# Kernel tuning notes

Measured on AMD Instinct MI355X. Metric: run time of the kernel, lower is better.

Reference implementation:

```python
import jax, jax.numpy as jnp
import numpy as np

EPS = 1e-5


def _gcn_conv(x, src, dst, norm, W, b, n_nodes):
    # PyG GCNConv: transform, then normalized scatter-add aggregation (self-loops included in src/dst)
    h = x @ W                                   # [N, out]
    msg = h[src] * norm[:, None]                # gather over edges [E+N, out]
    agg = jax.ops.segment_sum(msg, dst, num_segments=n_nodes)
    return agg + b


def _bn(x, gamma, beta):
    # BatchNorm1d in training mode: batch stats over node axis, biased variance
    mu = jnp.mean(x, axis=0)
    var = jnp.mean((x - mu) ** 2, axis=0)
    return (x - mu) * jax.lax.rsqrt(var + EPS) * gamma + beta


def setup_inputs() -> dict:
    key = jax.random.key(0)
    ks = jax.random.split(key, 8)
    N, E, F_in, H, F_out = 50000, 800000, 32, 96, 2
    x = jax.random.normal(ks[0], (N, F_in), dtype=jnp.float32)
    edge_index = jax.random.randint(ks[1], (2, E), 0, N, dtype=jnp.int64)
    def lin(k, fi, fo):
        s = 1.0 / np.sqrt(fi)
        return jax.random.uniform(k, (fi, fo), jnp.float32, -s, s)
    W1 = lin(ks[2], F_in, H); b1 = jnp.zeros((H,), jnp.float32)
    W2 = lin(ks[3], H, H);    b2 = jnp.zeros((H,), jnp.float32)
    W3 = lin(ks[4], H, H);    b3 = jnp.zeros((H,), jnp.float32)
    W4 = lin(ks[5], H, F_out); b4 = jnp.zeros((F_out,), jnp.float32)
    g1 = jnp.ones((H,), jnp.float32); be1 = jnp.zeros((H,), jnp.float32)
    g2 = jnp.ones((H,), jnp.float32); be2 = jnp.zeros((H,), jnp.float32)
    g3 = jnp.ones((H,), jnp.float32); be3 = jnp.zeros((H,), jnp.float32)
    return dict(x=x, edge_index=edge_index,
                W1=W1, b1=b1, g1=g1, be1=be1,
                W2=W2, b2=b2, g2=g2, be2=be2,
                W3=W3, b3=b3, g3=g3, be3=be3,
                W4=W4, b4=b4)


def reference(x, edge_index, W1, b1, g1, be1, W2, b2, g2, be2, W3, b3, g3, be3, W4, b4):
    N = x.shape[0]
    loop = jnp.arange(N, dtype=edge_index.dtype)
    src = jnp.concatenate([edge_index[0], loop])   # add self-loops
    dst = jnp.concatenate([edge_index[1], loop])
    deg = jax.ops.segment_sum(jnp.ones_like(dst, dtype=x.dtype), dst, num_segments=N)
    dinv = jnp.where(deg > 0, jax.lax.rsqrt(deg), 0.0)
    norm = dinv[src] * dinv[dst]                   # D^{-1/2} (A+I) D^{-1/2}

    h = jax.nn.relu(_bn(_gcn_conv(x, src, dst, norm, W1, b1, N), g1, be1))
    h = jax.nn.relu(_bn(_gcn_conv(h, src, dst, norm, W2, b2, N), g2, be2))
    h = jax.nn.relu(_bn(_gcn_conv(h, src, dst, norm, W3, b3, N), g3, be3))
    return _gcn_conv(h, src, dst, norm, W4, b4, N)
```

## Files before the change

kernel.cpp:

```cpp
#include <hip/hip_runtime.h>
#include <hip/hip_bf16.h>

using bf16x8 = __attribute__((ext_vector_type(8))) short;
using f32x4  = __attribute__((ext_vector_type(4))) float;

#define FS_CHUNK 4096

__device__ __forceinline__ float ldf(const void* p, size_t i, float isf){
  if (isf > 0.5f) return ((const float*)p)[i];
  unsigned int u = ((unsigned int)((const unsigned short*)p)[i]) << 16;
  return __uint_as_float(u);
}
__device__ __forceinline__ unsigned short f2bf(float v){
  unsigned int u = __float_as_uint(v);
  u = (u + 0x7FFFu + ((u >> 16) & 1u)) >> 16;
  return (unsigned short)u;
}
__device__ __forceinline__ unsigned int pk2(float a, float b){
  return (unsigned int)f2bf(a) | ((unsigned int)f2bf(b) << 16);
}
__device__ __forceinline__ float lo16(unsigned int u){ return __uint_as_float(u << 16); }
__device__ __forceinline__ float hi16(unsigned int u){ return __uint_as_float(u & 0xFFFF0000u); }

template<typename IT>
__device__ __forceinline__ void load8idx(const IT* p, int* o){
  if (sizeof(IT) == 2){
    uint4 v = *(const uint4*)p;
    o[0] = (int)(v.x & 0xFFFFu); o[1] = (int)(v.x >> 16);
    o[2] = (int)(v.y & 0xFFFFu); o[3] = (int)(v.y >> 16);
    o[4] = (int)(v.z & 0xFFFFu); o[5] = (int)(v.z >> 16);
    o[6] = (int)(v.w & 0xFFFFu); o[7] = (int)(v.w >> 16);
  } else {
    int4 a = ((const int4*)p)[0];
    int4 c = ((const int4*)p)[1];
    o[0]=a.x; o[1]=a.y; o[2]=a.z; o[3]=a.w;
    o[4]=c.x; o[5]=c.y; o[6]=c.z; o[7]=c.w;
  }
}

__global__ void k_fill(unsigned short* o, unsigned short v, int n){
  int i = blockIdx.x*blockDim.x + threadIdx.x;
  if (i < n) o[i] = v;
}

__global__ void k_prep(const unsigned short* xh, const unsigned int* eu,
                       float* flag, int nelemX, long long E,
                       const void* W1, const void* W2, const void* W3, const void* W4,
                       unsigned short* __restrict__ Wt1, unsigned short* __restrict__ Wt2,
                       unsigned short* __restrict__ Wt3, float* __restrict__ W4f,
                       int* __restrict__ cnt, float* __restrict__ stAll,
                       unsigned short* __restrict__ HS, int n){
  int t = threadIdx.x;
  if (blockIdx.x > 0){
    if (blockIdx.x == 1 && t < 96) HS[(size_t)96*n + t] = 0;
    int total = n + 4609;
    for (int i = (int)(blockIdx.x-1)*256 + t; i < total; i += (int)(gridDim.x-1)*256){
      if (i < n) cnt[i] = 0; else stAll[i - n] = 0.f;
    }
    return;
  }
  __shared__ int sf32, si64;
  __shared__ float sisf;
  if (t == 0){ sf32 = 0; si64 = 1; }
  __syncthreads();
  {
    int i = 2*t;
    if (i < nelemX){
      unsigned e8 = (xh[i] >> 7) & 0xFFu;
      if (e8 >= 140u) sf32 = 1;
    }
    if ((long long)(2*t + 1) < 2*E){
      if (eu[2*t + 1] != 0u) si64 = 0;
    }
  }
  __syncthreads();
  if (t == 0){
    flag[0] = (float)sf32; flag[1] = (float)si64;
    sisf = (float)sf32;
  }
  __syncthreads();
  float isf = sisf;
  for (int q = t; q < 3072; q += 256){
    int nn = q >> 5, k = q & 31;
    Wt1[q] = f2bf(ldf(W1, (size_t)96*k + nn, isf));
  }
  for (int q = t; q < 9216; q += 256){
    int nn = q/96, k = q - 96*nn;
    Wt2[q] = f2bf(ldf(W2, (size_t)96*k + nn, isf));
    Wt3[q] = f2bf(ldf(W3, (size_t)96*k + nn, isf));
  }
  if (t < 192) W4f[t] = ldf(W4, t, isf);
}

__global__ void k_cnt2p(const int* __restrict__ ei, const float* __restrict__ flag,
                        int* __restrict__ cnt, unsigned int* __restrict__ ec,
                        long long E, int n){
  long long i = (long long)blockIdx.x*blockDim.x + threadIdx.x;
  long long i0 = 2*i;
  if (i0 >= E) return;
  bool i64 = (flag[1] > 0.5f);
  bool two = (i0 + 1 < E);
  int s0, d0, s1 = 0, d1 = -1;
  if ((E & 1LL) == 0){
    if (i64){
      uint4 vs = ((const uint4*)ei)[i];
      uint4 vd = ((const uint4*)(ei + 2*E))[i];
      s0 = (int)vs.x; s1 = (int)vs.z; d0 = (int)vd.x; d1 = (int)vd.z;
    } else {
      int2 vs = ((const int2*)ei)[i];
      int2 vd = ((const int2*)(ei + E))[i];
      s0 = vs.x; s1 = vs.y; d0 = vd.x; d1 = vd.y;
    }
  } else {
    if (i64){ s0 = ei[2*i0]; d0 = ei[2*E + 2*i0];
              if (two){ s1 = ei[2*i0+2]; d1 = ei[2*E + 2*i0 + 2]; } }
    else    { s0 = ei[i0];   d0 = ei[E + i0];
              if (two){ s1 = ei[i0+1];   d1 = ei[E + i0 + 1]; } }
  }
  bool ok0 = ((unsigned)s0 < (unsigned)n) && ((unsigned)d0 < (unsigned)n);
  bool ok1 = two && ((unsigned)s1 < (unsigned)n) && ((unsigned)d1 < (unsigned)n);
  unsigned p0 = ok0 ? (((unsigned)d0 << 16) | (unsigned)s0) : 0xFFFFFFFFu;
  unsigned p1 = ok1 ? (((unsigned)d1 << 16) | (unsigned)s1) : 0xFFFFFFFFu;
  if (two){
    uint2 o; o.x = p0; o.y = p1;
    ((uint2*)ec)[i] = o;
  } else {
    ec[i0] = p0;
  }
  if (ok0) atomicAdd(&cnt[d0], 1);
  if (ok1) atomicAdd(&cnt[d1], 1);
}

__global__ void k_cnt2(const int* __restrict__ ei, const float* __restrict__ flag,
                       int* __restrict__ cnt, int* __restrict__ ec,
                       long long E, int n){
  long long i = (long long)blockIdx.x*blockDim.x + threadIdx.x;
  long long i0 = 2*i;
  if (i0 >= E) return;
  bool i64 = (flag[1] > 0.5f);
  bool two = (i0 + 1 < E);
  int s0, d0, s1 = 0, d1 = -1;
  if ((E & 1LL) == 0){
    if (i64){
      uint4 vs = ((const uint4*)ei)[i];
      uint4 vd = ((const uint4*)(ei + 2*E))[i];
      s0 = (int)vs.x; s1 = (int)vs.z; d0 = (int)vd.x; d1 = (int)vd.z;
    } else {
      int2 vs = ((const int2*)ei)[i];
      int2 vd = ((const int2*)(ei + E))[i];
      s0 = vs.x; s1 = vs.y; d0 = vd.x; d1 = vd.y;
    }
  } else {
    if (i64){ s0 = ei[2*i0]; d0 = ei[2*E + 2*i0];
              if (two){ s1 = ei[2*i0+2]; d1 = ei[2*E + 2*i0 + 2]; } }
    else    { s0 = ei[i0];   d0 = ei[E + i0];
              if (two){ s1 = ei[i0+1];   d1 = ei[E + i0 + 1]; } }
  }
  bool ok0 = ((unsigned)s0 < (unsigned)n) && ((unsigned)d0 < (unsigned)n);
  bool ok1 = two && ((unsigned)s1 < (unsigned)n) && ((unsigned)d1 < (unsigned)n);
  if (!ok0){ s0 = -1; d0 = -1; }
  if (!ok1){ s1 = -1; d1 = -1; }
  if (two){
    int4 o; o.x = s0; o.y = d0; o.z = s1; o.w = d1;
    ((int4*)ec)[i] = o;
  } else {
    int2 o; o.x = s0; o.y = d0;
    ((int2*)ec)[i0] = o;
  }
  if (ok0) atomicAdd(&cnt[d0], 1);
  if (ok1) atomicAdd(&cnt[d1], 1);
}

template<typename IT>
__global__ void k_emit2(const int* __restrict__ cnt, int* __restrict__ gctr,
                        int* __restrict__ rowst, int* __restrict__ cursor,
                        float* __restrict__ dinv, IT* __restrict__ csr, int n){
  int i = blockIdx.x*256 + threadIdx.x;
  int lane = threadIdx.x & 63;
  int v  = (i < n) ? cnt[i] : 0;
  int rv = (v + 7) & ~7;
  int s = rv;
  #pragma unroll
  for (int off = 1; off < 64; off <<= 1){
    int u = __shfl_up(s, off, 64);
    if (lane >= off) s += u;
  }
  int wtot = __shfl(s, 63, 64);
  int base = 0;
  if (lane == 63) base = atomicAdd(gctr, wtot);
  base = __shfl(base, 63, 64);
  if (i < n){
    int r = base + s - rv;
    rowst[i]  = r;
    cursor[i] = r;
    dinv[i]   = rsqrtf((float)(1 + v));
    for (int p = r + v; p < r + rv; ++p) csr[p] = (IT)n;
  }
}

__global__ __launch_bounds__(256) void k_fxp(const unsigned int* __restrict__ ec,
      int* __restrict__ cursor, unsigned short* __restrict__ csr,
      long long E, int n, int gF8,
      const void* __restrict__ x, const float* __restrict__ flag,
      const float* __restrict__ dinv, unsigned short* __restrict__ XS){
  int t = threadIdx.x;
  if ((int)blockIdx.x < gF8){
    int part = blockIdx.x & 7;
    long long base = (long long)(blockIdx.x >> 3) * FS_CHUNK;
    int pl = (int)(((long long)n *  part     ) >> 3);
    int pr = (int)(((long long)n * (part + 1)) >> 3);
    long long lim = base + FS_CHUNK < E ? base + FS_CHUNK : E;
    for (long long i = base + 4*t; i < lim; i += 1024){
      uint4 v = ((const uint4*)ec)[i >> 2];
      { int d = (int)(v.x >> 16);
        if (d >= pl && d < pr){ int p = atomicAdd(&cursor[d], 1); csr[p] = (unsigned short)(v.x & 0xFFFFu); } }
      if (i + 1 < lim){ int d = (int)(v.y >> 16);
        if (d >= pl && d < pr){ int p = atomicAdd(&cursor[d], 1); csr[p] = (unsigned short)(v.y & 0xFFFFu); } }
      if (i + 2 < lim){ int d = (int)(v.z >> 16);
        if (d >= pl && d < pr){ int p = atomicAdd(&cursor[d], 1); csr[p] = (unsigned short)(v.z & 0xFFFFu); } }
      if (i + 3 < lim){ int d = (int)(v.w >> 16);
        if (d >= pl && d < pr){ int p = atomicAdd(&cursor[d], 1); csr[p] = (unsigned short)(v.w & 0xFFFFu); } }
    }
    return;
  }
  int q = (int)(blockIdx.x - gF8)*256 + t;
  if (q < 4*(n+1)){
    int node = q >> 2, part = q & 3;
    uint4 o;
    if (node < n){
      float isf = flag[0];
      float di = dinv[node];
      if (isf > 0.5f){
        const float* xr = (const float*)x + (size_t)32*node + 8*part;
        o.x = pk2(xr[0]*di, xr[1]*di); o.y = pk2(xr[2]*di, xr[3]*di);
        o.z = pk2(xr[4]*di, xr[5]*di); o.w = pk2(xr[6]*di, xr[7]*di);
      } else {
        uint4 v = ((const uint4*)x)[(size_t)4*node + part];
        o.x = pk2(lo16(v.x)*di, hi16(v.x)*di);
        o.y = pk2(lo16(v.y)*di, hi16(v.y)*di);
        o.z = pk2(lo16(v.z)*di, hi16(v.z)*di);
        o.w = pk2(lo16(v.w)*di, hi16(v.w)*di);
      }
    } else { o.x = o.y = o.z = o.w = 0u; }
    ((uint4*)XS)[q] = o;
  }
}

__global__ __launch_bounds__(256) void k_fx(const int* __restrict__ ec,
      int* __restrict__ cursor, int* __restrict__ csr,
      long long E, int n, int gF8,
      const void* __restrict__ x, const float* __restrict__ flag,
      const float* __restrict__ dinv, unsigned short* __restrict__ XS){
  int t = threadIdx.x;
  if ((int)blockIdx.x < gF8){
    int part = blockIdx.x & 7;
    long long base = (long long)(blockIdx.x >> 3) * FS_CHUNK;
    int pl = (int)(((long long)n *  part     ) >> 3);
    int pr = (int)(((long long)n * (part + 1)) >> 3);
    long long lim = base + FS_CHUNK < E ? base + FS_CHUNK : E;
    for (long long i = base + 2*t; i < lim; i += 512){
      int4 v = ((const int4*)ec)[i >> 1];
      if (v.y >= pl && v.y < pr && (unsigned)v.x < (unsigned)n){
        int p = atomicAdd(&cursor[v.y], 1);
        csr[p] = v.x;
      }
      if (i + 1 < lim && v.w >= pl && v.w < pr && (unsigned)v.z < (unsigned)n){
        int p = atomicAdd(&cursor[v.w], 1);
        csr[p] = v.z;
      }
    }
    return;
  }
  int q = (int)(blockIdx.x - gF8)*256 + t;
  if (q < 4*(n+1)){
    int node = q >> 2, part = q & 3;
    uint4 o;
    if (node < n){
      float isf = flag[0];
      float di = dinv[node];
      if (isf > 0.5f){
        const float* xr = (const float*)x + (size_t)32*node + 8*part;
        o.x = pk2(xr[0]*di, xr[1]*di); o.y = pk2(xr[2]*di, xr[3]*di);
        o.z = pk2(xr[4]*di, xr[5]*di); o.w = pk2(xr[6]*di, xr[7]*di);
      } else {
        uint4 v = ((const uint4*)x)[(size_t)4*node + part];
        o.x = pk2(lo16(v.x)*di, hi16(v.x)*di);
        o.y = pk2(lo16(v.y)*di, hi16(v.y)*di);
        o.z = pk2(lo16(v.z)*di, hi16(v.z)*di);
        o.w = pk2(lo16(v.w)*di, hi16(v.w)*di);
      }
    } else { o.x = o.y = o.z = o.w = 0u; }
    ((uint4*)XS)[q] = o;
  }
}

#define ACC8(v) { a0+=lo16((v).x); a1+=hi16((v).x); a2+=lo16((v).y); a3+=hi16((v).y); \
                  a4+=lo16((v).z); a5+=hi16((v).z); a6+=lo16((v).w); a7+=hi16((v).w); }

template<typename IT>
__global__ __launch_bounds__(256) void k_aggx(const uint4* __restrict__ xs4,
      const int* __restrict__ rowst, const int* __restrict__ cnt,
      const IT* __restrict__ csr, const float* __restrict__ dinv,
      const unsigned short* __restrict__ Wt1b,
      unsigned short* __restrict__ Zb, float* __restrict__ stout, int n){
  __shared__ __align__(16) unsigned short Xs[64][40];
  __shared__ __align__(16) unsigned short Wt[96][40];
  __shared__ float bs[96], bq[96];
  int t = threadIdx.x;
  for (int q = t; q < 384; q += 256){
    uint4 v = ((const uint4*)Wt1b)[q];
    *(uint4*)&Wt[q >> 2][(q & 3)*8] = v;
  }
  if (t < 96){ bs[t] = 0.f; bq[t] = 0.f; }
  int g = t & 3, ty = t >> 2;
  int node = blockIdx.x*64 + ty;
  float a0=0.f,a1=0.f,a2=0.f,a3=0.f,a4=0.f,a5=0.f,a6=0.f,a7=0.f;
  if (node < n){
    uint4 v = xs4[(size_t)node*4 + g];
    ACC8(v);
    int bq_ = rowst[node];
    int bnd = bq_ + ((cnt[node] + 7) & ~7);
    for (int j = bq_; j < bnd; j += 8){
      int ix[8];
      load8idx<IT>(csr + j, ix);
      uint4 v0 = xs4[(size_t)ix[0]*4 + g];
      uint4 v1 = xs4[(size_t)ix[1]*4 + g];
      uint4 v2 = xs4[(size_t)ix[2]*4 + g];
      uint4 v3 = xs4[(size_t)ix[3]*4 + g];
      uint4 v4 = xs4[(size_t)ix[4]*4 + g];
      uint4 v5 = xs4[(size_t)ix[5]*4 + g];
      uint4 v6 = xs4[(size_t)ix[6]*4 + g];
      uint4 v7 = xs4[(size_t)ix[7]*4 + g];
      ACC8(v0); ACC8(v1); ACC8(v2); ACC8(v3);
      ACC8(v4); ACC8(v5); ACC8(v6); ACC8(v7);
    }
    float di = dinv[node];
    a0*=di; a1*=di; a2*=di; a3*=di; a4*=di; a5*=di; a6*=di; a7*=di;
  }
  uint4 o;
  o.x = pk2(a0,a1); o.y = pk2(a2,a3); o.z = pk2(a4,a5); o.w = pk2(a6,a7);
  *(uint4*)&Xs[ty][8*g] = o;
  __syncthreads();
  int wv = t >> 6, lane = t & 63;
  int m = lane & 15, quad = lane >> 4;
  bf16x8 av = *(const bf16x8*)&Xs[16*wv + m][8*quad];
  f32x4 acc[6];
  #pragma unroll
  for (int c = 0; c < 6; ++c) acc[c] = (f32x4)(0.f);
  #pragma unroll
  for (int c = 0; c < 6; ++c){
    bf16x8 bv = *(const bf16x8*)&Wt[16*c + m][8*quad];
    acc[c] = __builtin_amdgcn_mfma_f32_16x16x32_bf16(av, bv, acc[c], 0, 0, 0);
  }
  int rowbase = blockIdx.x*64 + 16*wv + 4*quad;
  #pragma unroll
  for (int c = 0; c < 6; ++c){
    int col = 16*c + m;
    float s = 0.f, q = 0.f;
    #pragma unroll
    for (int r = 0; r < 4; ++r){
      int rr = rowbase + r;
      if (rr < n){
        unsigned short h = f2bf(acc[c][r]);
        Zb[(size_t)96*rr + col] = h;
        float br = __uint_as_float(((unsigned int)h) << 16);
        s += br; q += br*br;
      }
    }
    atomicAdd(&bs[col], s);
    atomicAdd(&bq[col], q);
  }
  __syncthreads();
  if (t < 96){
    int rep = blockIdx.x & 7;
    atomicAdd(&stout[192*rep + t],      bs[t]);
    atomicAdd(&stout[192*rep + 96 + t], bq[t]);
  }
}

template<typename IT>
__global__ __launch_bounds__(192) void k_agg(const uint4* __restrict__ hsr,
      const int* __restrict__ rowst, const int* __restrict__ cnt,
      const IT* __restrict__ csr,
      const float* __restrict__ dinv, uint4* __restrict__ zb4,
      float* __restrict__ stout, int n){
  __shared__ float ls[16][97], lq[16][97];
  int g = threadIdx.x, ty = threadIdx.y;
  int t = ty*12 + g;
  int node = blockIdx.x*16 + ty;
  float r[8];
  if (node < n){
    uint4 v = hsr[(size_t)node*12 + g];
    float a0 = lo16(v.x), a1 = hi16(v.x), a2 = lo16(v.y), a3 = hi16(v.y);
    float a4 = lo16(v.z), a5 = hi16(v.z), a6 = lo16(v.w), a7 = hi16(v.w);
    int bq_ = rowst[node];
    int bnd = bq_ + ((cnt[node] + 7) & ~7);
    for (int j = bq_; j < bnd; j += 8){
      int ix[8];
      load8idx<IT>(csr + j, ix);
      uint4 v0 = hsr[(size_t)ix[0]*12 + g];
      uint4 v1 = hsr[(size_t)ix[1]*12 + g];
      uint4 v2 = hsr[(size_t)ix[2]*12 + g];
      uint4 v3 = hsr[(size_t)ix[3]*12 + g];
      uint4 v4 = hsr[(size_t)ix[4]*12 + g];
      uint4 v5 = hsr[(size_t)ix[5]*12 + g];
      uint4 v6 = hsr[(size_t)ix[6]*12 + g];
      uint4 v7 = hsr[(size_t)ix[7]*12 + g];
      ACC8(v0); ACC8(v1); ACC8(v2); ACC8(v3);
      ACC8(v4); ACC8(v5); ACC8(v6); ACC8(v7);
    }
    float di = dinv[node];
    uint4 o;
    o.x = pk2(a0*di, a1*di);
    o.y = pk2(a2*di, a3*di);
    o.z = pk2(a4*di, a5*di);
    o.w = pk2(a6*di, a7*di);
    zb4[(size_t)node*12 + g] = o;
    r[0]=lo16(o.x); r[1]=hi16(o.x); r[2]=lo16(o.y); r[3]=hi16(o.y);
    r[4]=lo16(o.z); r[5]=hi16(o.z); r[6]=lo16(o.w); r[7]=hi16(o.w);
  } else {
    #pragma unroll
    for (int jj = 0; jj < 8; ++jj) r[jj] = 0.f;
  }
  #pragma unroll
  for (int jj = 0; jj < 8; ++jj){
    ls[ty][8*g + jj] = r[jj];
    lq[ty][8*g + jj] = r[jj]*r[jj];
  }
  __syncthreads();
  if (t < 96){
    float s = 0.f, q = 0.f;
    #pragma unroll
    for (int rr = 0; rr < 16; ++rr){ s += ls[rr][t]; q += lq[rr][t]; }
    int rep = blockIdx.x & 7;
    atomicAdd(&stout[192*rep + t],      s);
    atomicAdd(&stout[192*rep + 96 + t], q);
  }
}

__global__ __launch_bounds__(256) void k_linm(const unsigned short* __restrict__ zb,
      const unsigned short* __restrict__ Wtb, const float* __restrict__ st,
      const void* __restrict__ gam, const void* __restrict__ bet,
      const float* __restrict__ flag, const float* __restrict__ dinv,
      unsigned short* __restrict__ HS, int n, float invN){
  __shared__ float sa[96], sc[96];
  __shared__ __align__(16) unsigned short Ys[64][104];
  __shared__ __align__(16) unsigned short Wt[96][104];
  int t = threadIdx.x;
  if (t < 96){
    float ssum = 0.f, qsum = 0.f;
    #pragma unroll
    for (int r = 0; r < 8; ++r){ ssum += st[192*r + t]; qsum += st[192*r + 96 + t]; }
    float isf = flag[0];
    float mu  = ssum*invN;
    float var = fmaxf(qsum*invN - mu*mu, 0.f);
    float istd = rsqrtf(var + 1e-5f);
    float a = ldf(gam, t, isf)*istd;
    sa[t] = a; sc[t] = ldf(bet, t, isf) - mu*a;
  }
  for (int q = t; q < 1152; q += 256){
    uint4 v = ((const uint4*)Wtb)[q];
    *(uint4*)&Wt[q/12][8*(q - 12*(q/12))] = v;
  }
  __syncthreads();
  {
    int row = t >> 2, part = t & 3;
    int node = blockIdx.x*64 + row;
    if (node < n){
      const uint4* zr = (const uint4*)(zb + (size_t)96*node) + 3*part;
      #pragma unroll
      for (int q = 0; q < 3; ++q){
        uint4 zz = zr[q];
        int k = 24*part + 8*q;
        float y0 = fmaxf(lo16(zz.x)*sa[k]   + sc[k],   0.f);
        float y1 = fmaxf(hi16(zz.x)*sa[k+1] + sc[k+1], 0.f);
        float y2 = fmaxf(lo16(zz.y)*sa[k+2] + sc[k+2], 0.f);
        float y3 = fmaxf(hi16(zz.y)*sa[k+3] + sc[k+3], 0.f);
        float y4 = fmaxf(lo16(zz.z)*sa[k+4] + sc[k+4], 0.f);
        float y5 = fmaxf(hi16(zz.z)*sa[k+5] + sc[k+5], 0.f);
        float y6 = fmaxf(lo16(zz.w)*sa[k+6] + sc[k+6], 0.f);
        float y7 = fmaxf(hi16(zz.w)*sa[k+7] + sc[k+7], 0.f);
        *(unsigned int*)&Ys[row][k]     = pk2(y0, y1);
        *(unsigned int*)&Ys[row][k + 2] = pk2(y2, y3);
        *(unsigned int*)&Ys[row][k + 4] = pk2(y4, y5);
        *(unsigned int*)&Ys[row][k + 6] = pk2(y6, y7);
      }
    } else {
      unsigned int* yp = (unsigned int*)&Ys[row][24*part];
      #pragma unroll
      for (int q = 0; q < 12; ++q) yp[q] = 0u;
    }
  }
  __syncthreads();
  int wv = t >> 6, lane = t & 63;
  int m = lane & 15, quad = lane >> 4;
  bf16x8 av[3];
  #pragma unroll
  for (int kt = 0; kt < 3; ++kt)
    av[kt] = *(const bf16x8*)&Ys[16*wv + m][32*kt + 8*quad];
  f32x4 acc[6];
  #pragma unroll
  for (int c = 0; c < 6; ++c) acc[c] = (f32x4)(0.f);
  #pragma unroll
  for (int c = 0; c < 6; ++c){
    const unsigned short* wrow = &Wt[16*c + m][8*quad];
    #pragma unroll
    for (int kt = 0; kt < 3; ++kt){
      bf16x8 bv = *(const bf16x8*)(wrow + 32*kt);
      acc[c] = __builtin_amdgcn_mfma_f32_16x16x32_bf16(av[kt], bv, acc[c], 0, 0, 0);
    }
  }
  int rowbase = blockIdx.x*64 + 16*wv + 4*quad;
  float div[4];
  #pragma unroll
  for (int r = 0; r < 4; ++r){ int rr = rowbase + r; div[r] = (rr < n) ? dinv[rr] : 0.f; }
  #pragma unroll
  for (int c = 0; c < 6; ++c){
    int col = 16*c + m;
    #pragma unroll
    for (int r = 0; r < 4; ++r){
      int rr = rowbase + r;
      if (rr < n) HS[(size_t)96*rr + col] = f2bf(acc[c][r]*div[r]);
    }
  }
}

__global__ __launch_bounds__(256) void k_lin4(const unsigned short* __restrict__ zb,
      const float* __restrict__ Wf, const float* __restrict__ st,
      const void* __restrict__ gam, const void* __restrict__ bet,
      const float* __restrict__ flag, const float* __restrict__ dinv,
      float* __restrict__ hs2, int n, float invN){
  __shared__ float sa[96], sc[96];
  int t = threadIdx.x;
  if (t < 96){
    float ssum = 0.f, qsum = 0.f;
    #pragma unroll
    for (int r = 0; r < 8; ++r){ ssum += st[192*r + t]; qsum += st[192*r + 96 + t]; }
    float isf = flag[0];
    float mu  = ssum*invN;
    float var = fmaxf(qsum*invN - mu*mu, 0.f);
    float istd = rsqrtf(var + 1e-5f);
    float a = ldf(gam, t, isf)*istd;
    sa[t] = a; sc[t] = ldf(bet, t, isf) - mu*a;
  }
  __syncthreads();
  int i = blockIdx.x*blockDim.x + t;
  if (i >= n) return;
  const uint4* zr = (const uint4*)(zb + (size_t)96*i);
  float a0 = 0.f, a1 = 0.f;
  #pragma unroll
  for (int q = 0; q < 12; ++q){
    uint4 zz = zr[q];
    int k = 8*q;
    float y;
    y = fmaxf(lo16(zz.x)*sa[k]   + sc[k],   0.f); a0 += y*Wf[2*k];    a1 += y*Wf[2*k+1];
    y = fmaxf(hi16(zz.x)*sa[k+1] + sc[k+1], 0.f); a0 += y*Wf[2*k+2];  a1 += y*Wf[2*k+3];
    y = fmaxf(lo16(zz.y)*sa[k+2] + sc[k+2], 0.f); a0 += y*Wf[2*k+4];  a1 += y*Wf[2*k+5];
    y = fmaxf(hi16(zz.y)*sa[k+3] + sc[k+3], 0.f); a0 += y*Wf[2*k+6];  a1 += y*Wf[2*k+7];
    y = fmaxf(lo16(zz.z)*sa[k+4] + sc[k+4], 0.f); a0 += y*Wf[2*k+8];  a1 += y*Wf[2*k+9];
    y = fmaxf(hi16(zz.z)*sa[k+5] + sc[k+5], 0.f); a0 += y*Wf[2*k+10]; a1 += y*Wf[2*k+11];
    y = fmaxf(lo16(zz.w)*sa[k+6] + sc[k+6], 0.f); a0 += y*Wf[2*k+12]; a1 += y*Wf[2*k+13];
    y = fmaxf(hi16(zz.w)*sa[k+7] + sc[k+7], 0.f); a0 += y*Wf[2*k+14]; a1 += y*Wf[2*k+15];
  }
  float di = dinv[i];
  hs2[(size_t)2*i]   = di*a0;
  hs2[(size_t)2*i+1] = di*a1;
}

template<typename IT>
__global__ void k_agg2(const float2* __restrict__ hs2, const int* __restrict__ rowst,
                       const int* __restrict__ cnt, const IT* __restrict__ csr,
                       const float* __restrict__ dinv,
                       const void* __restrict__ b4, const float* __restrict__ flag,
                       void* __restrict__ out, int n){
  int node = blockIdx.x*blockDim.x + threadIdx.x;
  if (node >= n) return;
  float2 a = hs2[node];
  int b = rowst[node], e = b + cnt[node];
  int j = b;
  for (; j + 3 < e; j += 4){
    float2 v0 = hs2[(size_t)csr[j]];
    float2 v1 = hs2[(size_t)csr[j+1]];
    float2 v2 = hs2[(size_t)csr[j+2]];
    float2 v3 = hs2[(size_t)csr[j+3]];
    a.x += v0.x + v1.x + v2.x + v3.x;
    a.y += v0.y + v1.y + v2.y + v3.y;
  }
  for (; j < e; ++j){
    float2 v = hs2[(size_t)csr[j]];
    a.x += v.x; a.y += v.y;
  }
  float isf = flag[0];
  float di = dinv[node];
  float v0 = a.x*di + ldf(b4, 0, isf);
  float v1 = a.y*di + ldf(b4, 1, isf);
  if (isf > 0.5f){
    ((float*)out)[(size_t)2*node]   = v0;
    ((float*)out)[(size_t)2*node+1] = v1;
  } else {
    ((unsigned short*)out)[(size_t)2*node]   = f2bf(v0);
    ((unsigned short*)out)[(size_t)2*node+1] = f2bf(v1);
  }
}

extern "C" void kernel_launch(void* const* d_in, const int* in_sizes, int n_in,
                              void* d_out, int out_size, void* d_ws, size_t ws_size,
                              hipStream_t stream)
{
  const int B = 256;
  unsigned short* outh = (unsigned short*)d_out;

  if (n_in < 16){
    k_fill<<<(out_size+B-1)/B, B, 0, stream>>>(outh, 0x3F40u, out_size); return;
  }
  const int N = in_sizes[0] / 32;
  const long long E = in_sizes[1] / 2;
  if (in_sizes[0] % 32 != 0 || out_size != 2*N){
    k_fill<<<(out_size+B-1)/B, B, 0, stream>>>(outh, 0x3F60u, out_size); return;
  }
  const bool u16 = (N < 65536);

  size_t Npad = ((size_t)N + 3) & ~(size_t)3;
  float* ws   = (float*)d_ws;
  float* dinv = ws;
  float* hs2  = dinv + Npad;
  float* flag = hs2 + (size_t)2*N;
  float* stAll= flag + 4;
  float* W4f  = stAll + 4612;
  unsigned short* Wt1b = (unsigned short*)(W4f + 192);
  unsigned short* Wt2b = Wt1b + 3072;
  unsigned short* Wt3b = Wt2b + 9216;
  int* cnt    = (int*)(Wt3b + 9216);
  int* cursor = cnt + N;
  int* rowst  = cursor + N;
  uintptr_t cs_ = (uintptr_t)(rowst + N);
  cs_ = (cs_ + 15) & ~(uintptr_t)15;
  void* csrv  = (void*)cs_;
  size_t csrCap = (size_t)E + 8*(size_t)N;
  size_t csrBytes = csrCap * (u16 ? 2 : 4);
  uintptr_t hp_ = cs_ + csrBytes;
  hp_ = (hp_ + 15) & ~(uintptr_t)15;
  unsigned short* HS = (unsigned short*)hp_;
  unsigned short* Zb = HS + (size_t)96*(N+1);
  uintptr_t ec_ = (uintptr_t)(Zb + (size_t)96*N);
  ec_ = (ec_ + 15) & ~(uintptr_t)15;
  void* ecv = (void*)ec_;

  size_t ecBytes = u16 ? ((size_t)E + 4)*4 : ((size_t)2*E + 4)*4;
  size_t needB = (ec_ + ecBytes - (uintptr_t)d_ws) + 64;
  if (ws_size < needB){
    k_fill<<<(out_size+B-1)/B, B, 0, stream>>>(outh, 0x3F00u, out_size); return;
  }

  unsigned short* XS = HS;

  const void* x  = d_in[0];
  const int*  ei = (const int*)d_in[1];
  const void* W1 = d_in[2];
  const void* g1 = d_in[4];  const void* be1 = d_in[5];
  const void* W2 = d_in[6];
  const void* g2 = d_in[8];  const void* be2 = d_in[9];
  const void* W3 = d_in[10];
  const void* g3 = d_in[12]; const void* be3 = d_in[13];
  const void* W4 = d_in[14];
  const void* b4 = d_in[15];

  float* stA = stAll;
  float* stB = stAll + 1536;
  float* stC = stAll + 3072;
  int*   gctr = (int*)(stAll + 4608);

  int gN  = (N + B - 1)/B;
  long long hE = (E + 1)/2;
  int gE2 = (int)((hE + B - 1)/B); if (gE2 < 1) gE2 = 1;
  int nb  = (N + 255)/256;
  int gA  = (N + 15)/16;
  int gL  = (N + 63)/64;
  int gXS = (4*(N+1) + 255)/256;
  int gF8 = (int)((E + FS_CHUNK - 1)/FS_CHUNK) * 8;
  float invN = 1.0f / (float)N;
  dim3 ablk(12,16);

  k_prep<<<33, B, 0, stream>>>((const unsigned short*)x, (const unsigned int*)ei,
                               flag, in_sizes[0], E, W1, W2, W3, W4,
                               Wt1b, Wt2b, Wt3b, W4f, cnt, stAll, HS, N);

  if (u16){
    unsigned short* csr = (unsigned short*)csrv;
    unsigned int* ec = (unsigned int*)ecv;
    k_cnt2p<<<gE2, B, 0, stream>>>(ei, flag, cnt, ec, E, N);
    k_emit2<unsigned short><<<nb, B, 0, stream>>>(cnt, gctr, rowst, cursor, dinv, csr, N);
    k_fxp<<<gF8 + gXS, B, 0, stream>>>(ec, cursor, csr, E, N, gF8, x, flag, dinv, XS);
    k_aggx<unsigned short><<<gL, B, 0, stream>>>((const uint4*)XS, rowst, cnt, csr, dinv, Wt1b, Zb, stA, N);
    k_linm<<<gL, B, 0, stream>>>(Zb, Wt2b, stA, g1, be1, flag, dinv, HS, N, invN);
    k_agg<unsigned short><<<gA, ablk, 0, stream>>>((const uint4*)HS, rowst, cnt, csr, dinv, (uint4*)Zb, stB, N);
    k_linm<<<gL, B, 0, stream>>>(Zb, Wt3b, stB, g2, be2, flag, dinv, HS, N, invN);
    k_agg<unsigned short><<<gA, ablk, 0, stream>>>((const uint4*)HS, rowst, cnt, csr, dinv, (uint4*)Zb, stC, N);
    k_lin4<<<gN, B, 0, stream>>>(Zb, W4f, stC, g3, be3, flag, dinv, hs2, N, invN);
    k_agg2<unsigned short><<<gN, B, 0, stream>>>((const float2*)hs2, rowst, cnt, csr, dinv, b4, flag, d_out, N);
  } else {
    int* csr = (int*)csrv;
    int* ec = (int*)ecv;
    k_cnt2<<<gE2, B, 0, stream>>>(ei, flag, cnt, ec, E, N);
    k_emit2<int><<<nb, B, 0, stream>>>(cnt, gctr, rowst, cursor, dinv, csr, N);
    k_fx<<<gF8 + gXS, B, 0, stream>>>(ec, cursor, csr, E, N, gF8, x, flag, dinv, XS);
    k_aggx<int><<<gL, B, 0, stream>>>((const uint4*)XS, rowst, cnt, csr, dinv, Wt1b, Zb, stA, N);
    k_linm<<<gL, B, 0, stream>>>(Zb, Wt2b, stA, g1, be1, flag, dinv, HS, N, invN);
    k_agg<int><<<gA, ablk, 0, stream>>>((const uint4*)HS, rowst, cnt, csr, dinv, (uint4*)Zb, stB, N);
    k_linm<<<gL, B, 0, stream>>>(Zb, Wt3b, stB, g2, be2, flag, dinv, HS, N, invN);
    k_agg<int><<<gA, ablk, 0, stream>>>((const uint4*)HS, rowst, cnt, csr, dinv, (uint4*)Zb, stC, N);
    k_lin4<<<gN, B, 0, stream>>>(Zb, W4f, stC, g3, be3, flag, dinv, hs2, N, invN);
    k_agg2<int><<<gN, B, 0, stream>>>((const float2*)hs2, rowst, cnt, csr, dinv, b4, flag, d_out, N);
  }
}
```

Baseline: 324.0 us.

## Bucket nodes by padded degree and process aggregation in degree-sorted order

Builds a histogram of padded node degrees in the emit pass, prefix-sums it in a tiny kernel, and scatters node ids into a degree-bucketed permutation inside the fill kernel. The aggregation kernels then map rows through this permutation so nodes with similar degree share a wavefront. The aim is to cut divergence from uneven per-node edge loops. The cost is an extra launch, atomics per node, and non-contiguous output writes and gathers through perm.

Result: slower. 1.071 ms (+230.5%).

```diff
diff --git a/kernel.cpp b/kernel.cpp
--- a/kernel.cpp
+++ b/kernel.cpp
@@ -53,7 +53,7 @@
   int t = threadIdx.x;
   if (blockIdx.x > 0){
     if (blockIdx.x == 1 && t < 96) HS[(size_t)96*n + t] = 0;
-    int total = n + 4609;
+    int total = n + 4676;
     for (int i = (int)(blockIdx.x-1)*256 + t; i < total; i += (int)(gridDim.x-1)*256){
       if (i < n) cnt[i] = 0; else stAll[i - n] = 0.f;
     }
@@ -174,7 +174,8 @@
 template<typename IT>
 __global__ void k_emit2(const int* __restrict__ cnt, int* __restrict__ gctr,
                         int* __restrict__ rowst, int* __restrict__ cursor,
-                        float* __restrict__ dinv, IT* __restrict__ csr, int n){
+                        float* __restrict__ dinv, IT* __restrict__ csr,
+                        int* __restrict__ bhist, int n){
   int i = blockIdx.x*256 + threadIdx.x;
   int lane = threadIdx.x & 63;
   int v  = (i < n) ? cnt[i] : 0;
@@ -195,14 +196,29 @@
     cursor[i] = r;
     dinv[i]   = rsqrtf((float)(1 + v));
     for (int p = r + v; p < r + rv; ++p) csr[p] = (IT)n;
-  }
+    int bk = rv >> 3; if (bk > 63) bk = 63;
+    atomicAdd(&bhist[bk], 1);
+  }
+}
+
+__global__ void k_bpre(const int* __restrict__ bhist, int* __restrict__ bcur){
+  int t = threadIdx.x;
+  int h = bhist[t];
+  int s = h;
+  #pragma unroll
+  for (int off = 1; off < 64; off <<= 1){
+    int u = __shfl_up(s, off, 64);
+    if (t >= off) s += u;
+  }
+  bcur[t] = s - h;
 }
 
 __global__ __launch_bounds__(256) void k_fxp(const unsigned int* __restrict__ ec,
       int* __restrict__ cursor, unsigned short* __restrict__ csr,
-      long long E, int n, int gF8,
+      long long E, int n, int gF8, int gXS,
       const void* __restrict__ x, const float* __restrict__ flag,
-      const float* __restrict__ dinv, unsigned short* __restrict__ XS){
+      const float* __restrict__ dinv, unsigned short* __restrict__ XS,
+      const int* __restrict__ cnt, int* __restrict__ bcur, int* __restrict__ perm){
   int t = threadIdx.x;
   if ((int)blockIdx.x < gF8){
     int part = blockIdx.x & 7;
@@ -223,34 +239,44 @@
     }
     return;
   }
-  int q = (int)(blockIdx.x - gF8)*256 + t;
-  if (q < 4*(n+1)){
-    int node = q >> 2, part = q & 3;
-    uint4 o;
-    if (node < n){
-      float isf = flag[0];
-      float di = dinv[node];
-      if (isf > 0.5f){
-        const float* xr = (const float*)x + (size_t)32*node + 8*part;
-        o.x = pk2(xr[0]*di, xr[1]*di); o.y = pk2(xr[2]*di, xr[3]*di);
-        o.z = pk2(xr[4]*di, xr[5]*di); o.w = pk2(xr[6]*di, xr[7]*di);
-      } else {
-        uint4 v = ((const uint4*)x)[(size_t)4*node + part];
-        o.x = pk2(lo16(v.x)*di, hi16(v.x)*di);
-        o.y = pk2(lo16(v.y)*di, hi16(v.y)*di);
-        o.z = pk2(lo16(v.z)*di, hi16(v.z)*di);
-        o.w = pk2(lo16(v.w)*di, hi16(v.w)*di);
-      }
-    } else { o.x = o.y = o.z = o.w = 0u; }
-    ((uint4*)XS)[q] = o;
+  if ((int)blockIdx.x < gF8 + gXS){
+    int q = (int)(blockIdx.x - gF8)*256 + t;
+    if (q < 4*(n+1)){
+      int node = q >> 2, part = q & 3;
+      uint4 o;
+      if (node < n){
+        float isf = flag[0];
+        float di = dinv[node];
+        if (isf > 0.5f){
+          const float* xr = (const float*)x + (size_t)32*node + 8*part;
+          o.x = pk2(xr[0]*di, xr[1]*di); o.y = pk2(xr[2]*di, xr[3]*di);
+          o.z = pk2(xr[4]*di, xr[5]*di); o.w = pk2(xr[6]*di, xr[7]*di);
+        } else {
+          uint4 v = ((const uint4*)x)[(size_t)4*node + part];
+          o.x = pk2(lo16(v.x)*di, hi16(v.x)*di);
+          o.y = pk2(lo16(v.y)*di, hi16(v.y)*di);
+          o.z = pk2(lo16(v.z)*di, hi16(v.z)*di);
+          o.w = pk2(lo16(v.w)*di, hi16(v.w)*di);
+        }
+      } else { o.x = o.y = o.z = o.w = 0u; }
+      ((uint4*)XS)[q] = o;
+    }
+    return;
+  }
+  int i = (int)(blockIdx.x - gF8 - gXS)*256 + t;
+  if (i < n){
+    int bk = ((cnt[i] + 7) & ~7) >> 3; if (bk > 63) bk = 63;
+    int pos = atomicAdd(&bcur[bk], 1);
+    perm[pos] = i;
   }
 }
 
 __global__ __launch_bounds__(256) void k_fx(const int* __restrict__ ec,
       int* __restrict__ cursor, int* __restrict__ csr,
-      long long E, int n, int gF8,
+      long long E, int n, int gF8, int gXS,
       const void* __restrict__ x, const float* __restrict__ flag,
-      const float* __restrict__ dinv, unsigned short* __restrict__ XS){
+      const float* __restrict__ dinv, unsigned short* __restrict__ XS,
+      const int* __restrict__ cnt, int* __restrict__ bcur, int* __restrict__ perm){
   int t = threadIdx.x;
   if ((int)blockIdx.x < gF8){
     int part = blockIdx.x & 7;
@@ -271,26 +297,35 @@
     }
     return;
   }
-  int q = (int)(blockIdx.x - gF8)*256 + t;
-  if (q < 4*(n+1)){
-    int node = q >> 2, part = q & 3;
-    uint4 o;
-    if (node < n){
-      float isf = flag[0];
-      float di = dinv[node];
-      if (isf > 0.5f){
-        const float* xr = (const float*)x + (size_t)32*node + 8*part;
-        o.x = pk2(xr[0]*di, xr[1]*di); o.y = pk2(xr[2]*di, xr[3]*di);
-        o.z = pk2(xr[4]*di, xr[5]*di); o.w = pk2(xr[6]*di, xr[7]*di);
-      } else {
-        uint4 v = ((const uint4*)x)[(size_t)4*node + part];
-        o.x = pk2(lo16(v.x)*di, hi16(v.x)*di);
-        o.y = pk2(lo16(v.y)*di, hi16(v.y)*di);
-        o.z = pk2(lo16(v.z)*di, hi16(v.z)*di);
-        o.w = pk2(lo16(v.w)*di, hi16(v.w)*di);
-      }
-    } else { o.x = o.y = o.z = o.w = 0u; }
-    ((uint4*)XS)[q] = o;
+  if ((int)blockIdx.x < gF8 + gXS){
+    int q = (int)(blockIdx.x - gF8)*256 + t;
+    if (q < 4*(n+1)){
+      int node = q >> 2, part = q & 3;
+      uint4 o;
+      if (node < n){
+        float isf = flag[0];
+        float di = dinv[node];
+        if (isf > 0.5f){
+          const float* xr = (const float*)x + (size_t)32*node + 8*part;
+          o.x = pk2(xr[0]*di, xr[1]*di); o.y = pk2(xr[2]*di, xr[3]*di);
+          o.z = pk2(xr[4]*di, xr[5]*di); o.w = pk2(xr[6]*di, xr[7]*di);
+        } else {
+          uint4 v = ((const uint4*)x)[(size_t)4*node + part];
+          o.x = pk2(lo16(v.x)*di, hi16(v.x)*di);
+          o.y = pk2(lo16(v.y)*di, hi16(v.y)*di);
+          o.z = pk2(lo16(v.z)*di, hi16(v.z)*di);
+          o.w = pk2(lo16(v.w)*di, hi16(v.w)*di);
+        }
+      } else { o.x = o.y = o.z = o.w = 0u; }
+      ((uint4*)XS)[q] = o;
+    }
+    return;
+  }
+  int i = (int)(blockIdx.x - gF8 - gXS)*256 + t;
+  if (i < n){
+    int bk = ((cnt[i] + 7) & ~7) >> 3; if (bk > 63) bk = 63;
+    int pos = atomicAdd(&bcur[bk], 1);
+    perm[pos] = i;
   }
 }
 
@@ -300,7 +335,8 @@
 template<typename IT>
 __global__ __launch_bounds__(256) void k_aggx(const uint4* __restrict__ xs4,
       const int* __restrict__ rowst, const int* __restrict__ cnt,
-      const IT* __restrict__ csr, const float* __restrict__ dinv,
+      const IT* __restrict__ csr, const int* __restrict__ perm,
+      const float* __restrict__ dinv,
       const unsigned short* __restrict__ Wt1b,
       unsigned short* __restrict__ Zb, float* __restrict__ stout, int n){
   __shared__ __align__(16) unsigned short Xs[64][40];
@@ -313,9 +349,10 @@
   }
   if (t < 96){ bs[t] = 0.f; bq[t] = 0.f; }
   int g = t & 3, ty = t >> 2;
-  int node = blockIdx.x*64 + ty;
+  int idx = blockIdx.x*64 + ty;
+  int node = (idx < n) ? perm[idx] : -1;
   float a0=0.f,a1=0.f,a2=0.f,a3=0.f,a4=0.f,a5=0.f,a6=0.f,a7=0.f;
-  if (node < n){
+  if (node >= 0){
     uint4 v = xs4[(size_t)node*4 + g];
     ACC8(v);
     int bq_ = rowst[node];
@@ -353,16 +390,18 @@
     acc[c] = __builtin_amdgcn_mfma_f32_16x16x32_bf16(av, bv, acc[c], 0, 0, 0);
   }
   int rowbase = blockIdx.x*64 + 16*wv + 4*quad;
+  int nw[4];
+  #pragma unroll
+  for (int r = 0; r < 4; ++r){ int ii = rowbase + r; nw[r] = (ii < n) ? perm[ii] : -1; }
   #pragma unroll
   for (int c = 0; c < 6; ++c){
     int col = 16*c + m;
     float s = 0.f, q = 0.f;
     #pragma unroll
     for (int r = 0; r < 4; ++r){
-      int rr = rowbase + r;
-      if (rr < n){
+      if (nw[r] >= 0){
         unsigned short h = f2bf(acc[c][r]);
-        Zb[(size_t)96*rr + col] = h;
+        Zb[(size_t)96*nw[r] + col] = h;
         float br = __uint_as_float(((unsigned int)h) << 16);
         s += br; q += br*br;
       }
@@ -381,15 +420,16 @@
 template<typename IT>
 __global__ __launch_bounds__(192) void k_agg(const uint4* __restrict__ hsr,
       const int* __restrict__ rowst, const int* __restrict__ cnt,
-      const IT* __restrict__ csr,
+      const IT* __restrict__ csr, const int* __restrict__ perm,
       const float* __restrict__ dinv, uint4* __restrict__ zb4,
       float* __restrict__ stout, int n){
   __shared__ float ls[16][97], lq[16][97];
   int g = threadIdx.x, ty = threadIdx.y;
   int t = ty*12 + g;
-  int node = blockIdx.x*16 + ty;
+  int idx = blockIdx.x*16 + ty;
+  int node = (idx < n) ? perm[idx] : -1;
   float r[8];
-  if (node < n){
+  if (node >= 0){
     uint4 v = hsr[(size_t)node*12 + g];
     float a0 = lo16(v.x), a1 = hi16(v.x), a2 = lo16(v.y), a3 = hi16(v.y);
     float a4 = lo16(v.z), a5 = hi16(v.z), a6 = lo16(v.w), a7 = hi16(v.w);
@@ -626,14 +666,17 @@
   float* hs2  = dinv + Npad;
   float* flag = hs2 + (size_t)2*N;
   float* stAll= flag + 4;
-  float* W4f  = stAll + 4612;
+  int* bhist  = (int*)(stAll + 4612);
+  int* bcur   = (int*)(stAll + 4676);
+  float* W4f  = stAll + 4740;
   unsigned short* Wt1b = (unsigned short*)(W4f + 192);
   unsigned short* Wt2b = Wt1b + 3072;
   unsigned short* Wt3b = Wt2b + 9216;
   int* cnt    = (int*)(Wt3b + 9216);
   int* cursor = cnt + N;
   int* rowst  = cursor + N;
-  uintptr_t cs_ = (uintptr_t)(rowst + N);
+  int* perm   = rowst + N;
+  uintptr_t cs_ = (uintptr_t)(perm + N);
   cs_ = (cs_ + 15) & ~(uintptr_t)15;
   void* csrv  = (void*)cs_;
   size_t csrCap = (size_t)E + 8*(size_t)N;
@@ -677,6 +720,7 @@
   int gA  = (N + 15)/16;
   int gL  = (N + 63)/64;
   int gXS = (4*(N+1) + 255)/256;
+  int gPS = (N + 255)/256;
   int gF8 = (int)((E + FS_CHUNK - 1)/FS_CHUNK) * 8;
   float invN = 1.0f / (float)N;
   dim3 ablk(12,16);
@@ -689,26 +733,30 @@
     unsigned short* csr = (unsigned short*)csrv;
     unsigned int* ec = (unsigned int*)ecv;
     k_cnt2p<<<gE2, B, 0, stream>>>(ei, flag, cnt, ec, E, N);
-    k_emit2<unsigned short><<<nb, B, 0, stream>>>(cnt, gctr, rowst, cursor, dinv, csr, N);
-    k_fxp<<<gF8 + gXS, B, 0, stream>>>(ec, cursor, csr, E, N, gF8, x, flag, dinv, XS);
-    k_aggx<unsigned short><<<gL, B, 0, stream>>>((const uint4*)XS, rowst, cnt, csr, dinv, Wt1b, Zb, stA, N);
+    k_emit2<unsigned short><<<nb, B, 0, stream>>>(cnt, gctr, rowst, cursor, dinv, csr, bhist, N);
+    k_bpre<<<1, 64, 0, stream>>>(bhist, bcur);
+    k_fxp<<<gF8 + gXS + gPS, B, 0, stream>>>(ec, cursor, csr, E, N, gF8, gXS,
+                                             x, flag, dinv, XS, cnt, bcur, perm);
+    k_aggx<unsigned short><<<gL, B, 0, stream>>>((const uint4*)XS, rowst, cnt, csr, perm, dinv, Wt1b, Zb, stA, N);
     k_linm<<<gL, B, 0, stream>>>(Zb, Wt2b, stA, g1, be1, flag, dinv, HS, N, invN);
-    k_agg<unsigned short><<<gA, ablk, 0, stream>>>((const uint4*)HS, rowst, cnt, csr, dinv, (uint4*)Zb, stB, N);
+    k_agg<unsigned short><<<gA, ablk, 0, stream>>>((const uint4*)HS, rowst, cnt, csr, perm, dinv, (uint4*)Zb, stB, N);
     k_linm<<<gL, B, 0, stream>>>(Zb, Wt3b, stB, g2, be2, flag, dinv, HS, N, invN);
-    k_agg<unsigned short><<<gA, ablk, 0, stream>>>((const uint4*)HS, rowst, cnt, csr, dinv, (uint4*)Zb, stC, N);
+    k_agg<unsigned short><<<gA, ablk, 0, stream>>>((const uint4*)HS, rowst, cnt, csr, perm, dinv, (uint4*)Zb, stC, N);
     k_lin4<<<gN, B, 0, stream>>>(Zb, W4f, stC, g3, be3, flag, dinv, hs2, N, invN);
     k_agg2<unsigned short><<<gN, B, 0, stream>>>((const float2*)hs2, rowst, cnt, csr, dinv, b4, flag, d_out, N);
   } else {
     int* csr = (int*)csrv;
     int* ec = (int*)ecv;
     k_cnt2<<<gE2, B, 0, stream>>>(ei, flag, cnt, ec, E, N);
-    k_emit2<int><<<nb, B, 0, stream>>>(cnt, gctr, rowst, cursor, dinv, csr, N);
-    k_fx<<<gF8 + gXS, B, 0, stream>>>(ec, cursor, csr, E, N, gF8, x, flag, dinv, XS);
-    k_aggx<int><<<gL, B, 0, stream>>>((const uint4*)XS, rowst, cnt, csr, dinv, Wt1b, Zb, stA, N);
+    k_emit2<int><<<nb, B, 0, stream>>>(cnt, gctr, rowst, cursor, dinv, csr, bhist, N);
+    k_bpre<<<1, 64, 0, stream>>>(bhist, bcur);
+    k_fx<<<gF8 + gXS + gPS, B, 0, stream>>>(ec, cursor, csr, E, N, gF8, gXS,
+                                            x, flag, dinv, XS, cnt, bcur, perm);
+    k_aggx<int><<<gL, B, 0, stream>>>((const uint4*)XS, rowst, cnt, csr, perm, dinv, Wt1b, Zb, stA, N);
     k_linm<<<gL, B, 0, stream>>>(Zb, Wt2b, stA, g1, be1, flag, dinv, HS, N, invN);
-    k_agg<int><<<gA, ablk, 0, stream>>>((const uint4*)HS, rowst, cnt, csr, dinv, (uint4*)Zb, stB, N);
+    k_agg<int><<<gA, ablk, 0, stream>>>((const uint4*)HS, rowst, cnt, csr, perm, dinv, (uint4*)Zb, stB, N);
     k_linm<<<gL, B, 0, stream>>>(Zb, Wt3b, stB, g2, be2, flag, dinv, HS, N, invN);
-    k_agg<int><<<gA, ablk, 0, stream>>>((const uint4*)HS, rowst, cnt, csr, dinv, (uint4*)Zb, stC, N);
+    k_agg<int><<<gA, ablk, 0, stream>>>((const uint4*)HS, rowst, cnt, csr, perm, dinv, (uint4*)Zb, stC, N);
     k_lin4<<<gN, B, 0, stream>>>(Zb, W4f, stC, g3, be3, flag, dinv, hs2, N, invN);
     k_agg2<int><<<gN, B, 0, stream>>>((const float2*)hs2, rowst, cnt, csr, dinv, b4, flag, d_out, N);
   }
```
